# Kernel tuning notes

Hardware: AMD Instinct MI355X
Metric: run time of the kernel (lower is better)

The kernel has to match this reference:

```python
import jax, jax.numpy as jnp
import numpy as np

EMBED_DIM = 2048
N_HEADS = 16
D_HEAD = EMBED_DIM // N_HEADS


def setup_inputs() -> dict:
    key = jax.random.key(0)
    kx, kq, kk, kv = jax.random.split(key, 4)
    B, N, D = 4, 2048, EMBED_DIM
    x = jax.random.normal(kx, (B, N, D), dtype=jnp.float32)
    Wq = jax.random.normal(kq, (D, D), dtype=jnp.float32) * 0.02
    Wk = jax.random.normal(kk, (D, D), dtype=jnp.float32) * 0.02
    Wv = jax.random.normal(kv, (D, D), dtype=jnp.float32) * 0.02
    return {"x": x, "Wq": Wq, "Wk": Wk, "Wv": Wv}


def reference(x, Wq, Wk, Wv):
    # x: [B, N, D]; weights applied as x @ W (matching torch.matmul in source)
    B, N, D = x.shape
    H, d = N_HEADS, D_HEAD
    # [B, N, D] -> [B, H, N, d]
    Q = (x @ Wq).reshape(B, N, H, d).transpose(0, 2, 1, 3)
    K = (x @ Wk).reshape(B, N, H, d).transpose(0, 2, 1, 3)
    V = (x @ Wv).reshape(B, N, H, d).transpose(0, 2, 1, 3)
    scale = 1.0 / jnp.sqrt(jnp.asarray(d, dtype=x.dtype))
    # non-causal SDPA (torch default: no mask, scale = 1/sqrt(d_head))
    scores = jnp.einsum('bhqd,bhkd->bhqk', Q, K) * scale  # [B,H,N,N]
    attn = jax.nn.softmax(scores, axis=-1)
    out = jnp.einsum('bhqk,bhkd->bhqd', attn, V)  # [B,H,N,d]
    return out
```

## Files before the change

### kernel.cpp

```cpp
#include <hip/hip_runtime.h>
#include <hip/hip_bf16.h>

#define B 4
#define N 2048
#define D 2048
#define H 16
#define DH 128
#define NT 32

typedef unsigned short u16;
typedef __attribute__((ext_vector_type(8))) short short8;
typedef __attribute__((ext_vector_type(4))) float floatx4;

__device__ __forceinline__ u16 f2b(float f) {
    union { __hip_bfloat16 h; u16 u; } cv;
    cv.h = __float2bfloat16(f);
    return cv.u;
}

__device__ __forceinline__ floatx4 mfma16(short8 a, short8 b, floatx4 c) {
    return __builtin_amdgcn_mfma_f32_16x16x32_bf16(a, b, c, 0, 0, 0);
}

#if __has_builtin(__builtin_amdgcn_exp2f)
#define EXP2(x) __builtin_amdgcn_exp2f(x)
#else
#define EXP2(x) exp2f(x)
#endif

__device__ __forceinline__ void async16(const void* g, void* l) {
    __builtin_amdgcn_global_load_lds(
        (const __attribute__((address_space(1))) unsigned int*)g,
        (__attribute__((address_space(3))) unsigned int*)l, 16, 0, 0);
}

__global__ __launch_bounds__(256) void cvt_x(const float* __restrict__ x,
                                             u16* __restrict__ xb) {
    size_t i = ((size_t)blockIdx.x * 256 + threadIdx.x) * 8;
    float4 v0 = *(const float4*)&x[i];
    float4 v1 = *(const float4*)&x[i + 4];
    union { u16 u[8]; uint4 s; } pk;
    pk.u[0] = f2b(v0.x); pk.u[1] = f2b(v0.y); pk.u[2] = f2b(v0.z); pk.u[3] = f2b(v0.w);
    pk.u[4] = f2b(v1.x); pk.u[5] = f2b(v1.y); pk.u[6] = f2b(v1.z); pk.u[7] = f2b(v1.w);
    *(uint4*)&xb[i] = pk.s;
}

__global__ __launch_bounds__(256) void cvt_w_t(const float* __restrict__ Wq,
                                               const float* __restrict__ Wk,
                                               const float* __restrict__ Wv,
                                               u16* __restrict__ wt) {
    __shared__ float tile[64][65];
    const int z = blockIdx.z;
    const float* W = (z == 0) ? Wq : (z == 1) ? Wk : Wv;
    const float scl = (z == 0) ? 0.12751743342f : 1.0f;
    const int k0 = blockIdx.x * 64, n0 = blockIdx.y * 64;
    const int tr = threadIdx.x >> 4, tc = threadIdx.x & 15;
#pragma unroll
    for (int i = 0; i < 4; i++) {
        int kk = tr + 16 * i;
        float4 vv = *(const float4*)&W[(size_t)(k0 + kk) * D + n0 + tc * 4];
        tile[kk][tc * 4 + 0] = vv.x; tile[kk][tc * 4 + 1] = vv.y;
        tile[kk][tc * 4 + 2] = vv.z; tile[kk][tc * 4 + 3] = vv.w;
    }
    __syncthreads();
#pragma unroll
    for (int i = 0; i < 4; i++) {
        int nn = tr + 16 * i;
        union { u16 u[4]; ushort4 s; } pk;
#pragma unroll
        for (int j = 0; j < 4; j++) pk.u[j] = f2b(tile[tc * 4 + j][nn] * scl);
        *(ushort4*)&wt[(size_t)z * D * D + (size_t)(n0 + nn) * D + k0 + tc * 4] = pk.s;
    }
}

#define KT 32
__global__ __launch_bounds__(512, 2) void qkv_gemm(const u16* __restrict__ xb,
                                                   const u16* __restrict__ wt,
                                                   u16* __restrict__ qo,
                                                   u16* __restrict__ ko,
                                                   u16* __restrict__ vo) {
    __shared__ u16 lds[2][2][2][128 * 64];

    const int bid = blockIdx.x;
    const int swz = (bid & 7) * 96 + (bid >> 3);
    const int tm = swz & 31;
    const int tn = swz >> 5;

    const int t = threadIdx.x, lane = t & 63, w = t >> 6;
    const int wr = w >> 2, wc = w & 3;
    const int q4 = lane >> 4, lr = lane & 15;

    const int m0 = tm * 256;
    const int n0 = tn * 256;

    unsigned aoff[2][2], boff[2][2];
#pragma unroll
    for (int i = 0; i < 2; i++) {
        const int off = i * 8192 + w * 1024 + lane * 16;
        const int row = off >> 7;
        const int s = (off >> 4) & 7;
        const int col = ((s ^ (row & 7))) * 8;
#pragma unroll
        for (int h = 0; h < 2; h++) {
            aoff[h][i] = (unsigned)((m0 + h * 128 + row) * D + col);
            boff[h][i] = (unsigned)((n0 + h * 128 + row) * D + col);
        }
    }

#define STAGE_A(buf, h, j) {                                                        \
    async16(xb + aoff[h][0] + (unsigned)(j) * 64, (char*)&lds[buf][0][h][0] + w * 1024);        \
    async16(xb + aoff[h][1] + (unsigned)(j) * 64, (char*)&lds[buf][0][h][0] + 8192 + w * 1024); }
#define STAGE_B(buf, h, j) {                                                        \
    async16(wt + boff[h][0] + (unsigned)(j) * 64, (char*)&lds[buf][1][h][0] + w * 1024);        \
    async16(wt + boff[h][1] + (unsigned)(j) * 64, (char*)&lds[buf][1][h][0] + 8192 + w * 1024); }
#define BAR() __builtin_amdgcn_s_barrier()
#define LGKM0() asm volatile("s_waitcnt lgkmcnt(0)" ::: "memory")

    floatx4 acc[8][4];
#pragma unroll
    for (int i = 0; i < 8; i++)
#pragma unroll
        for (int j = 0; j < 4; j++) acc[i][j] = (floatx4){0.f, 0.f, 0.f, 0.f};

    STAGE_A(0, 0, 0); STAGE_A(0, 1, 0);
    STAGE_B(0, 0, 0); STAGE_B(0, 1, 0);
    STAGE_A(1, 0, 1); STAGE_A(1, 1, 1);
    asm volatile("s_waitcnt vmcnt(4)" ::: "memory");
    BAR();

    for (int g = 0; g < KT; g++) {
        const int cur = g & 1, nxt = cur ^ 1;
        short8 a0[4][2], a1[4][2], b0[2][2], b1[2][2];

#pragma unroll
        for (int mf = 0; mf < 4; mf++) {
            const int hrow = mf * 16 + lr;
            const int sw = hrow & 7;
#pragma unroll
            for (int ks = 0; ks < 2; ks++)
                a0[mf][ks] = *(const short8*)&lds[cur][0][wr][hrow * 64 + ((ks * 4 + q4) ^ sw) * 8];
        }
#pragma unroll
        for (int nf = 0; nf < 2; nf++) {
            const int hrow = (wc & 1) * 64 + nf * 16 + lr;
            const int sw = hrow & 7;
#pragma unroll
            for (int ks = 0; ks < 2; ks++)
                b0[nf][ks] = *(const short8*)&lds[cur][1][wc >> 1][hrow * 64 + ((ks * 4 + q4) ^ sw) * 8];
        }
        if (g + 1 < KT) STAGE_B(nxt, 0, g + 1);
        BAR();
        LGKM0();
        __builtin_amdgcn_s_setprio(1);
#pragma unroll
        for (int nf = 0; nf < 2; nf++)
#pragma unroll
            for (int mf = 0; mf < 4; mf++)
#pragma unroll
                for (int ks = 0; ks < 2; ks++)
                    acc[mf][nf] = mfma16(a0[mf][ks], b0[nf][ks], acc[mf][nf]);
        __builtin_amdgcn_s_setprio(0);
        BAR();

#pragma unroll
        for (int mf = 0; mf < 4; mf++) {
            const int hrow = 64 + mf * 16 + lr;
            const int sw = hrow & 7;
#pragma unroll
            for (int ks = 0; ks < 2; ks++)
                a1[mf][ks] = *(const short8*)&lds[cur][0][wr][hrow * 64 + ((ks * 4 + q4) ^ sw) * 8];
        }
        if (g + 1 < KT) STAGE_B(nxt, 1, g + 1);
        BAR();
        LGKM0();
        __builtin_amdgcn_s_setprio(1);
#pragma unroll
        for (int nf = 0; nf < 2; nf++)
#pragma unroll
            for (int mf = 0; mf < 4; mf++)
#pragma unroll
                for (int ks = 0; ks < 2; ks++)
                    acc[4 + mf][nf] = mfma16(a1[mf][ks], b0[nf][ks], acc[4 + mf][nf]);
        __builtin_amdgcn_s_setprio(0);
        BAR();

#pragma unroll
        for (int nf = 0; nf < 2; nf++) {
            const int hrow = (wc & 1) * 64 + (2 + nf) * 16 + lr;
            const int sw = hrow & 7;
#pragma unroll
            for (int ks = 0; ks < 2; ks++)
                b1[nf][ks] = *(const short8*)&lds[cur][1][wc >> 1][hrow * 64 + ((ks * 4 + q4) ^ sw) * 8];
        }
        if (g + 2 < KT) STAGE_A(cur, 0, g + 2);
        BAR();
        LGKM0();
        __builtin_amdgcn_s_setprio(1);
#pragma unroll
        for (int nf = 0; nf < 2; nf++)
#pragma unroll
            for (int mf = 0; mf < 4; mf++)
#pragma unroll
                for (int ks = 0; ks < 2; ks++)
                    acc[4 + mf][2 + nf] = mfma16(a1[mf][ks], b1[nf][ks], acc[4 + mf][2 + nf]);
        __builtin_amdgcn_s_setprio(0);
        BAR();

        if (g + 2 < KT) STAGE_A(cur, 1, g + 2);
        BAR();
        __builtin_amdgcn_s_setprio(1);
#pragma unroll
        for (int nf = 0; nf < 2; nf++)
#pragma unroll
            for (int mf = 0; mf < 4; mf++)
#pragma unroll
                for (int ks = 0; ks < 2; ks++)
                    acc[mf][2 + nf] = mfma16(a0[mf][ks], b1[nf][ks], acc[mf][2 + nf]);
        __builtin_amdgcn_s_setprio(0);
        if (g == KT - 2) { asm volatile("s_waitcnt vmcnt(0)" ::: "memory"); }
        else if (g < KT - 2) { asm volatile("s_waitcnt vmcnt(4)" ::: "memory"); }
        BAR();
    }

    const int z = tn >> 3;
    u16* dst = (z == 0) ? qo : (z == 1) ? ko : vo;
    const int c2b = (tn & 7) * 256 + wc * 64;
    const int grb = tm * 256 + wr * 128;
#pragma unroll
    for (int mf = 0; mf < 8; mf++)
#pragma unroll
        for (int nf = 0; nf < 4; nf++)
#pragma unroll
            for (int r = 0; r < 4; r++) {
                int gr = grb + mf * 16 + q4 * 4 + r;
                int c2 = c2b + nf * 16 + lr;
                int b_ = gr >> 11, n_ = gr & (N - 1);
                int head = c2 >> 7, dcol = c2 & 127;
                dst[((size_t)(b_ * H + head) * N + n_) * DH + dcol] = f2b(acc[mf][nf][r]);
            }
#undef STAGE_A
#undef STAGE_B
#undef BAR
#undef LGKM0
}

__global__ __launch_bounds__(256) void transpose_v(const u16* __restrict__ v,
                                                   u16* __restrict__ vt) {
    __shared__ u16 tile[64][72];
    const int bh = blockIdx.z;
    const int n0 = blockIdx.x * 64, d0 = blockIdx.y * 64;
    const int t = threadIdx.x;
#pragma unroll
    for (int i = 0; i < 2; i++) {
        int gid = t + 256 * i;
        int nl = gid >> 3, g = gid & 7;
        *(uint4*)&tile[nl][g * 8] =
            *(const uint4*)&v[((size_t)bh * N + n0 + nl) * DH + d0 + g * 8];
    }
    __syncthreads();
#pragma unroll
    for (int i = 0; i < 2; i++) {
        int gid = t + 256 * i;
        int dl = gid >> 3, gn = gid & 7;
        union { u16 u[8]; uint4 s; } pk;
#pragma unroll
        for (int j = 0; j < 8; j++) {
            int kp = gn * 8 + j;
            int src = 32 * (kp >> 5) + 16 * (kp & 1) + ((kp >> 1) & 15);
            pk.u[j] = tile[src][dl];
        }
        *(uint4*)&vt[((size_t)bh * DH + d0 + dl) * N + n0 + gn * 8] = pk.s;
    }
}

#define FMAX2 17.312340491f
__global__ __launch_bounds__(256, 2) void attn_kernel(const u16* __restrict__ q,
                                                      const u16* __restrict__ k,
                                                      const u16* __restrict__ vt,
                                                      float* __restrict__ out) {
    __shared__ u16 Ks[2][64][128];
    __shared__ u16 Vts[2][128][64];
    __shared__ u16 Ps[128][64];

    const int beta = blockIdx.x;
    const int bh = (beta & 7) + 8 * (beta >> 7);
    const int qt = (beta >> 3) & 15;
    const int t = threadIdx.x;
    const int w = t >> 6, lane = t & 63;
    const int half = lane >> 4, lr = lane & 15;
    const int a = w & 1, b = w >> 1;

    const size_t qbase = ((size_t)bh * N + (size_t)qt * 128) * DH;
    short8 af[4][4];
#pragma unroll
    for (int rt = 0; rt < 4; rt++)
#pragma unroll
        for (int ks = 0; ks < 4; ks++)
            af[rt][ks] = *(const short8*)&q[qbase + (size_t)(64 * b + 16 * rt + lr) * DH
                                            + ks * 32 + half * 8];

    float lrow[4][4];
    floatx4 o[4][4];
#pragma unroll
    for (int rt = 0; rt < 4; rt++)
#pragma unroll
        for (int r = 0; r < 4; r++) lrow[rt][r] = 0.f;
#pragma unroll
    for (int rt = 0; rt < 4; rt++)
#pragma unroll
        for (int ct = 0; ct < 4; ct++) o[rt][ct] = (floatx4){0.f, 0.f, 0.f, 0.f};

    const size_t kbase = (size_t)bh * N * DH;
    const size_t vtbase = (size_t)bh * DH * N;
    const u16* kp[4];
    const u16* vp[4];
#pragma unroll
    for (int c = 0; c < 4; c++) {
        int grp = 4 * w + c;
        int krow = 4 * grp + (lane >> 4);
        int kg = (lane & 15) ^ (krow & 15);
        kp[c] = &k[kbase + (size_t)krow * DH + kg * 8];
        int vrow = 8 * grp + (lane >> 3);
        int vg = (lane & 7) ^ (vrow & 7);
        vp[c] = &vt[vtbase + (size_t)vrow * N + vg * 8];
    }

#pragma unroll
    for (int c = 0; c < 4; c++) {
        async16(kp[c], (char*)&Ks[0][0][0] + (4 * w + c) * 1024);
        async16(vp[c], (char*)&Vts[0][0][0] + (4 * w + c) * 1024);
    }

    for (int kt = 0; kt < NT; kt++) {
        const int cur = kt & 1;
        __syncthreads();

        floatx4 sf[4][2];
#pragma unroll
        for (int ct = 0; ct < 2; ct++) {
            short8 bf[4];
#pragma unroll
            for (int ks = 0; ks < 4; ks++) {
                int gs = (4 * ks + half) ^ lr;
                bf[ks] = *(const short8*)&Ks[cur][32 * a + 16 * ct + lr][gs * 8];
            }
#pragma unroll
            for (int rt = 0; rt < 4; rt++) {
                floatx4 s = (floatx4){0.f, 0.f, 0.f, 0.f};
#pragma unroll
                for (int ks = 0; ks < 4; ks++) s = mfma16(af[rt][ks], bf[ks], s);
                sf[rt][ct] = s;
            }
        }

#pragma unroll
        for (int rt = 0; rt < 4; rt++)
#pragma unroll
            for (int r = 0; r < 4; r++) {
                int row = 64 * b + 16 * rt + 4 * half + r;
                float p0 = EXP2(sf[rt][0][r] - FMAX2);
                float p1 = EXP2(sf[rt][1][r] - FMAX2);
                lrow[rt][r] += p0 + p1;
                unsigned int pw = (unsigned int)f2b(p0) | ((unsigned int)f2b(p1) << 16);
                int u = (16 * a + lr) ^ ((row & 7) << 2);
                *(unsigned int*)&Ps[row][u * 2] = pw;
            }

        __syncthreads();

        if (kt + 1 < NT) {
            const int nb = cur ^ 1;
#pragma unroll
            for (int c = 0; c < 4; c++) {
                async16(kp[c] + (size_t)(kt + 1) * 64 * DH,
                        (char*)&Ks[nb][0][0] + (4 * w + c) * 1024);
                async16(vp[c] + (size_t)(kt + 1) * 64,
                        (char*)&Vts[nb][0][0] + (4 * w + c) * 1024);
            }
        }

#pragma unroll
        for (int ks = 0; ks < 2; ks++) {
            short8 a2[4];
#pragma unroll
            for (int rt = 0; rt < 4; rt++) {
                int g = (4 * ks + half) ^ (lr & 7);
                a2[rt] = *(const short8*)&Ps[64 * b + 16 * rt + lr][g * 8];
            }
#pragma unroll
            for (int ct = 0; ct < 4; ct++) {
                int dd = 64 * a + 16 * ct + lr;
                int gv = (4 * ks + half) ^ (lr & 7);
                short8 bv = *(const short8*)&Vts[cur][dd][gv * 8];
#pragma unroll
                for (int rt = 0; rt < 4; rt++)
                    o[rt][ct] = mfma16(a2[rt], bv, o[rt][ct]);
            }
        }
    }

    __syncthreads();
    float* Ls = (float*)&Ps[0][0];
#pragma unroll
    for (int rt = 0; rt < 4; rt++)
#pragma unroll
        for (int r = 0; r < 4; r++) {
            float s = lrow[rt][r];
            s += __shfl_xor(s, 1);
            s += __shfl_xor(s, 2);
            s += __shfl_xor(s, 4);
            s += __shfl_xor(s, 8);
            if (lr == 0) Ls[a * 128 + (64 * b + 16 * rt + 4 * half + r)] = s;
        }
    __syncthreads();
    const size_t obase = ((size_t)bh * N + (size_t)qt * 128) * DH;
#pragma unroll
    for (int rt = 0; rt < 4; rt++)
#pragma unroll
        for (int r = 0; r < 4; r++) {
            int row = 64 * b + 16 * rt + 4 * half + r;
            float inv = 1.f / (Ls[row] + Ls[128 + row]);
#pragma unroll
            for (int ct = 0; ct < 4; ct++)
                out[obase + (size_t)row * DH + 64 * a + 16 * ct + lr] = o[rt][ct][r] * inv;
        }
}

extern "C" void kernel_launch(void* const* d_in, const int* in_sizes, int n_in,
                              void* d_out, int out_size, void* d_ws, size_t ws_size,
                              hipStream_t stream) {
    const float* x  = (const float*)d_in[0];
    const float* Wq = (const float*)d_in[1];
    const float* Wk = (const float*)d_in[2];
    const float* Wv = (const float*)d_in[3];
    float* out = (float*)d_out;
    char* ws = (char*)d_ws;

    u16* xb = (u16*)(ws);
    u16* wt = (u16*)(ws + 33554432);
    u16* qb = (u16*)(ws + 58720256);
    u16* kb = (u16*)(ws + 92274688);
    u16* vb = (u16*)(ws + 125829120);
    u16* vtb = (u16*)(ws);

    cvt_x<<<dim3(8192), dim3(256), 0, stream>>>(x, xb);
    cvt_w_t<<<dim3(32, 32, 3), dim3(256), 0, stream>>>(Wq, Wk, Wv, wt);
    qkv_gemm<<<dim3(768), dim3(512), 0, stream>>>(xb, wt, qb, kb, vb);
    transpose_v<<<dim3(32, 2, 64), dim3(256), 0, stream>>>(vb, vtb);
    attn_kernel<<<dim3(1024), dim3(256), 0, stream>>>(qb, kb, vtb, out);
}
```

Before: 499.2 us.

## Restructure QKV GEMM main loop to fewer barriers and new tile swizzle

Reorders the QKV GEMM inner loop: all A/B fragments for a K step are read from LDS up front, the B prefetch for the next step is issued at the top, and the A prefetch is batched after a single mid-iteration barrier. This cuts the per-iteration barriers from about eight to two and drops the explicit lgkmcnt waits. It also replaces the block-to-tile swizzle with a grouped mapping over 8 chunks, aiming at better L2 reuse. In exchange, more fragments stay live in registers at once. The A prefetch into the current buffer now relies on a single barrier to order it after every wave's LDS reads.

```diff
diff --git a/kernel.cpp b/kernel.cpp
--- a/kernel.cpp
+++ b/kernel.cpp
@@ -82,9 +82,10 @@
     __shared__ u16 lds[2][2][2][128 * 64];
 
     const int bid = blockIdx.x;
-    const int swz = (bid & 7) * 96 + (bid >> 3);
-    const int tm = swz & 31;
-    const int tn = swz >> 5;
+    const int c = bid & 7, i = bid >> 3;
+    const int i6 = (i * 43) >> 8;
+    const int tm = ((c >> 2) << 4) + i6;
+    const int tn = (c & 3) * 6 + (i - 6 * i6);
 
     const int t = threadIdx.x, lane = t & 63, w = t >> 6;
     const int wr = w >> 2, wc = w & 3;
@@ -95,15 +96,15 @@
 
     unsigned aoff[2][2], boff[2][2];
 #pragma unroll
-    for (int i = 0; i < 2; i++) {
-        const int off = i * 8192 + w * 1024 + lane * 16;
+    for (int ii = 0; ii < 2; ii++) {
+        const int off = ii * 8192 + w * 1024 + lane * 16;
         const int row = off >> 7;
         const int s = (off >> 4) & 7;
         const int col = ((s ^ (row & 7))) * 8;
 #pragma unroll
         for (int h = 0; h < 2; h++) {
-            aoff[h][i] = (unsigned)((m0 + h * 128 + row) * D + col);
-            boff[h][i] = (unsigned)((n0 + h * 128 + row) * D + col);
+            aoff[h][ii] = (unsigned)((m0 + h * 128 + row) * D + col);
+            boff[h][ii] = (unsigned)((n0 + h * 128 + row) * D + col);
         }
     }
 
@@ -114,13 +115,12 @@
     async16(wt + boff[h][0] + (unsigned)(j) * 64, (char*)&lds[buf][1][h][0] + w * 1024);        \
     async16(wt + boff[h][1] + (unsigned)(j) * 64, (char*)&lds[buf][1][h][0] + 8192 + w * 1024); }
 #define BAR() __builtin_amdgcn_s_barrier()
-#define LGKM0() asm volatile("s_waitcnt lgkmcnt(0)" ::: "memory")
 
     floatx4 acc[8][4];
 #pragma unroll
-    for (int i = 0; i < 8; i++)
-#pragma unroll
-        for (int j = 0; j < 4; j++) acc[i][j] = (floatx4){0.f, 0.f, 0.f, 0.f};
+    for (int x = 0; x < 8; x++)
+#pragma unroll
+        for (int j = 0; j < 4; j++) acc[x][j] = (floatx4){0.f, 0.f, 0.f, 0.f};
 
     STAGE_A(0, 0, 0); STAGE_A(0, 1, 0);
     STAGE_B(0, 0, 0); STAGE_B(0, 1, 0);
@@ -130,8 +130,10 @@
 
     for (int g = 0; g < KT; g++) {
         const int cur = g & 1, nxt = cur ^ 1;
+
+        if (g + 1 < KT) { STAGE_B(nxt, 0, g + 1); STAGE_B(nxt, 1, g + 1); }
+
         short8 a0[4][2], a1[4][2], b0[2][2], b1[2][2];
-
 #pragma unroll
         for (int mf = 0; mf < 4; mf++) {
             const int hrow = mf * 16 + lr;
@@ -148,9 +150,23 @@
             for (int ks = 0; ks < 2; ks++)
                 b0[nf][ks] = *(const short8*)&lds[cur][1][wc >> 1][hrow * 64 + ((ks * 4 + q4) ^ sw) * 8];
         }
-        if (g + 1 < KT) STAGE_B(nxt, 0, g + 1);
-        BAR();
-        LGKM0();
+#pragma unroll
+        for (int mf = 0; mf < 4; mf++) {
+            const int hrow = 64 + mf * 16 + lr;
+            const int sw = hrow & 7;
+#pragma unroll
+            for (int ks = 0; ks < 2; ks++)
+                a1[mf][ks] = *(const short8*)&lds[cur][0][wr][hrow * 64 + ((ks * 4 + q4) ^ sw) * 8];
+        }
+#pragma unroll
+        for (int nf = 0; nf < 2; nf++) {
+            const int hrow = (wc & 1) * 64 + (2 + nf) * 16 + lr;
+            const int sw = hrow & 7;
+#pragma unroll
+            for (int ks = 0; ks < 2; ks++)
+                b1[nf][ks] = *(const short8*)&lds[cur][1][wc >> 1][hrow * 64 + ((ks * 4 + q4) ^ sw) * 8];
+        }
+
         __builtin_amdgcn_s_setprio(1);
 #pragma unroll
         for (int nf = 0; nf < 2; nf++)
@@ -160,19 +176,7 @@
                 for (int ks = 0; ks < 2; ks++)
                     acc[mf][nf] = mfma16(a0[mf][ks], b0[nf][ks], acc[mf][nf]);
         __builtin_amdgcn_s_setprio(0);
-        BAR();
-
-#pragma unroll
-        for (int mf = 0; mf < 4; mf++) {
-            const int hrow = 64 + mf * 16 + lr;
-            const int sw = hrow & 7;
-#pragma unroll
-            for (int ks = 0; ks < 2; ks++)
-                a1[mf][ks] = *(const short8*)&lds[cur][0][wr][hrow * 64 + ((ks * 4 + q4) ^ sw) * 8];
-        }
-        if (g + 1 < KT) STAGE_B(nxt, 1, g + 1);
-        BAR();
-        LGKM0();
+
         __builtin_amdgcn_s_setprio(1);
 #pragma unroll
         for (int nf = 0; nf < 2; nf++)
@@ -182,19 +186,11 @@
                 for (int ks = 0; ks < 2; ks++)
                     acc[4 + mf][nf] = mfma16(a1[mf][ks], b0[nf][ks], acc[4 + mf][nf]);
         __builtin_amdgcn_s_setprio(0);
+
         BAR();
 
-#pragma unroll
-        for (int nf = 0; nf < 2; nf++) {
-            const int hrow = (wc & 1) * 64 + (2 + nf) * 16 + lr;
-            const int sw = hrow & 7;
-#pragma unroll
-            for (int ks = 0; ks < 2; ks++)
-                b1[nf][ks] = *(const short8*)&lds[cur][1][wc >> 1][hrow * 64 + ((ks * 4 + q4) ^ sw) * 8];
-        }
-        if (g + 2 < KT) STAGE_A(cur, 0, g + 2);
-        BAR();
-        LGKM0();
+        if (g + 2 < KT) { STAGE_A(cur, 0, g + 2); STAGE_A(cur, 1, g + 2); }
+
         __builtin_amdgcn_s_setprio(1);
 #pragma unroll
         for (int nf = 0; nf < 2; nf++)
@@ -203,12 +199,6 @@
 #pragma unroll
                 for (int ks = 0; ks < 2; ks++)
                     acc[4 + mf][2 + nf] = mfma16(a1[mf][ks], b1[nf][ks], acc[4 + mf][2 + nf]);
-        __builtin_amdgcn_s_setprio(0);
-        BAR();
-
-        if (g + 2 < KT) STAGE_A(cur, 1, g + 2);
-        BAR();
-        __builtin_amdgcn_s_setprio(1);
 #pragma unroll
         for (int nf = 0; nf < 2; nf++)
 #pragma unroll
@@ -217,9 +207,10 @@
                 for (int ks = 0; ks < 2; ks++)
                     acc[mf][2 + nf] = mfma16(a0[mf][ks], b1[nf][ks], acc[mf][2 + nf]);
         __builtin_amdgcn_s_setprio(0);
+
         if (g == KT - 2) { asm volatile("s_waitcnt vmcnt(0)" ::: "memory"); }
         else if (g < KT - 2) { asm volatile("s_waitcnt vmcnt(4)" ::: "memory"); }
-        BAR();
+        if (g + 1 < KT) BAR();
     }
 
     const int z = tn >> 3;
@@ -241,7 +232,6 @@
 #undef STAGE_A
 #undef STAGE_B
 #undef BAR
-#undef LGKM0
 }
 
 __global__ __launch_bounds__(256) void transpose_v(const u16* __restrict__ v,
```

After: 487.2 us. 2.4% less time.
